# Kernel tuning notes

Measured on AMD Instinct MI355X. Metric: run time of the kernel, lower is better.

## Reference

```python
import jax, jax.numpy as jnp
import numpy as np

USER_NUM = 100_000
ITEM_NUM = 50_000
N = USER_NUM + ITEM_NUM          # total nodes in the bipartite graph
HIDDEN = 64
LAYERS = 3
BATCH = 4096
NNZ = 4_800_000                  # ~avg degree 32


def setup_inputs() -> dict:
    key = jax.random.key(0)
    ks = jax.random.split(key, 7)
    emb = jax.random.normal(ks[0], (N, HIDDEN), dtype=jnp.float32) * 0.02
    rows = jax.random.randint(ks[1], (NNZ,), 0, N, dtype=jnp.int32)
    cols = jax.random.randint(ks[2], (NNZ,), 0, N, dtype=jnp.int32)
    # normalized-laplacian-like positive values, scaled ~ 1/avg_degree
    vals = jax.random.uniform(ks[3], (NNZ,), dtype=jnp.float32) * (1.0 / 32.0)
    user = jax.random.randint(ks[4], (BATCH,), 0, USER_NUM, dtype=jnp.int32)
    pos = jax.random.randint(ks[5], (BATCH,), USER_NUM, N, dtype=jnp.int32)
    neg = jax.random.randint(ks[6], (BATCH,), USER_NUM, N, dtype=jnp.int32)
    return {"emb": emb, "vals": vals, "rows": rows, "cols": cols,
            "user": user, "pos": pos, "neg": neg}


def _spmm(rows, cols, vals, x):
    # sparse [N,N] @ dense [N,d] in COO form: gather + scale + segment-sum
    return jax.ops.segment_sum(vals[:, None] * x[cols], rows, num_segments=N)


def reference(emb, vals, rows, cols, user, pos, neg):
    # layer-0 gathers
    user_acc = emb[user]
    pos_acc = emb[pos]
    neg_acc = emb[neg]
    e = emb
    for _ in range(LAYERS):
        e = _spmm(rows, cols, vals, e)
        user_acc = user_acc + e[user]
        pos_acc = pos_acc + e[pos]
        neg_acc = neg_acc + e[neg]
    denom = jnp.float32(LAYERS + 1)
    u = user_acc / denom   # mean over stacked layers
    p = pos_acc / denom
    n = neg_acc / denom
    pos_logits = jnp.einsum('id,id->i', u, p)
    neg_logits = jnp.einsum('id,id->i', u, n)
    # -log(sigmoid(x)) == -log_sigmoid(x) (numerically stable)
    loss = -jax.nn.log_sigmoid(pos_logits - neg_logits)
    return loss.sum()
```

## Files before the change

kernel.cpp:

```cpp
#include <hip/hip_runtime.h>

#define HIDDEN 64
#define PAD 96
#define CHUNK 8192
#define NBMAX 640
#define CAP 9600

typedef unsigned int uint;

__device__ __forceinline__ ushort f2bf(float f) {
    uint u = __float_as_uint(f);
    u = (u + 0x7FFFu + ((u >> 16) & 1u)) >> 16;
    return (ushort)u;
}
__device__ __forceinline__ float bf2f(ushort h) {
    return __uint_as_float(((uint)h) << 16);
}


__global__ void __launch_bounds__(256) k_f2bf(const float4* __restrict__ src,
                                              ushort* __restrict__ dst, int n4) {
    int i = blockIdx.x * blockDim.x + threadIdx.x;
    if (i >= n4) return;
    float4 f = src[i];
    ushort4 o;
    o.x = f2bf(f.x); o.y = f2bf(f.y); o.z = f2bf(f.z); o.w = f2bf(f.w);
    ((ushort4*)dst)[i] = o;
}


__global__ void __launch_bounds__(512) k_stage(const int* __restrict__ rows,
                                               const int* __restrict__ cols,
                                               const float* __restrict__ vals,
                                               int* __restrict__ cursor,
                                               int2* __restrict__ staged,
                                               int nnz, int nb) {
    __shared__ int  hS[NBMAX];
    __shared__ int  lsS[NBMAX];
    __shared__ int  gsS[NBMAX];
    __shared__ int  lcS[NBMAX];
    __shared__ int  ps[512];
    __shared__ int2 stg[CHUNK];

    int t  = threadIdx.x;
    int cb = blockIdx.x * CHUNK;

    for (int k = t; k < nb; k += 512) hS[k] = 0;
    __syncthreads();

    int4 ra[4];
    #pragma unroll
    for (int j = 0; j < 4; ++j) {
        int idx = cb + j * 2048 + t * 4;
        int4 r4;
        if (idx + 3 < nnz) {
            r4 = *(const int4*)(rows + idx);
        } else {
            r4.x = (idx     < nnz) ? rows[idx]     : -1;
            r4.y = (idx + 1 < nnz) ? rows[idx + 1] : -1;
            r4.z = (idx + 2 < nnz) ? rows[idx + 2] : -1;
            r4.w = (idx + 3 < nnz) ? rows[idx + 3] : -1;
        }
        ra[j] = r4;
        if (r4.x >= 0) atomicAdd(&hS[r4.x >> 8], 1);
        if (r4.y >= 0) atomicAdd(&hS[r4.y >> 8], 1);
        if (r4.z >= 0) atomicAdd(&hS[r4.z >> 8], 1);
        if (r4.w >= 0) atomicAdd(&hS[r4.w >> 8], 1);
    }
    __syncthreads();

    int k0 = 2 * t, k1 = 2 * t + 1;
    int c0 = (k0 < nb) ? hS[k0] : 0;
    int c1 = (k1 < nb) ? hS[k1] : 0;
    ps[t] = c0 + c1;
    __syncthreads();
    for (int d = 1; d < 512; d <<= 1) {
        int p = (t >= d) ? ps[t - d] : 0;
        __syncthreads();
        ps[t] += p;
        __syncthreads();
    }
    int excl = ps[t] - (c0 + c1);
    if (k0 < nb) {
        lsS[k0] = excl;
        gsS[k0] = atomicAdd(&cursor[k0], c0);
    }
    if (k1 < nb) {
        lsS[k1] = excl + c0;
        gsS[k1] = atomicAdd(&cursor[k1], c1);
    }
    __syncthreads();
    for (int k = t; k < nb; k += 512) lcS[k] = lsS[k];
    __syncthreads();

    #pragma unroll
    for (int j = 0; j < 4; ++j) {
        int idx = cb + j * 2048 + t * 4;
        int4 r4 = ra[j];
        int4 c4; float4 v4;
        if (idx + 3 < nnz) {
            c4 = *(const int4*)(cols + idx);
            v4 = *(const float4*)(vals + idx);
        } else {
            c4.x = (idx     < nnz) ? cols[idx]     : 0;
            c4.y = (idx + 1 < nnz) ? cols[idx + 1] : 0;
            c4.z = (idx + 2 < nnz) ? cols[idx + 2] : 0;
            c4.w = (idx + 3 < nnz) ? cols[idx + 3] : 0;
            v4.x = (idx     < nnz) ? vals[idx]     : 0.f;
            v4.y = (idx + 1 < nnz) ? vals[idx + 1] : 0.f;
            v4.z = (idx + 2 < nnz) ? vals[idx + 2] : 0.f;
            v4.w = (idx + 3 < nnz) ? vals[idx + 3] : 0.f;
        }
        if (r4.x >= 0) { int s = atomicAdd(&lcS[r4.x >> 8], 1);
            stg[s] = make_int2(c4.x | ((r4.x & 255) << 18), __float_as_int(v4.x)); }
        if (r4.y >= 0) { int s = atomicAdd(&lcS[r4.y >> 8], 1);
            stg[s] = make_int2(c4.y | ((r4.y & 255) << 18), __float_as_int(v4.y)); }
        if (r4.z >= 0) { int s = atomicAdd(&lcS[r4.z >> 8], 1);
            stg[s] = make_int2(c4.z | ((r4.z & 255) << 18), __float_as_int(v4.z)); }
        if (r4.w >= 0) { int s = atomicAdd(&lcS[r4.w >> 8], 1);
            stg[s] = make_int2(c4.w | ((r4.w & 255) << 18), __float_as_int(v4.w)); }
    }
    __syncthreads();

    int m_total = nnz - cb; if (m_total > CHUNK) m_total = CHUNK;
    for (int i = t; i < m_total; i += 512) {
        int2 e = stg[i];
        int lo = 0, hi = nb - 1;
        while (lo < hi) {
            int mid = (lo + hi + 1) >> 1;
            if (lsS[mid] <= i) lo = mid; else hi = mid - 1;
        }
        int k = lo;
        int pos = gsS[k] + (i - lsS[k]);
        if (pos < CAP) staged[(size_t)k * CAP + pos] = e;
    }
}

__global__ void __launch_bounds__(1024) k_fine(const int2* __restrict__ staged,
                                               const int* __restrict__ stagecnt,
                                               int2* __restrict__ pack,
                                               int* __restrict__ cnt, int n) {
    __shared__ int2 out[CAP];
    __shared__ int hist[256], rstart[256], cursor[256], s2[256];
    int k = blockIdx.x;
    int t = threadIdx.x;
    size_t s0 = (size_t)k * CAP;
    int ck = stagecnt[k]; if (ck > CAP) ck = CAP;
    if (t < 256) hist[t] = 0;
    __syncthreads();
    for (int i = t; i < ck; i += 1024)
        atomicAdd(&hist[((uint)staged[s0 + i].x) >> 18], 1);
    __syncthreads();
    if (t < 256) s2[t] = hist[t];
    __syncthreads();
    for (int d = 1; d < 256; d <<= 1) {
        int p = (t < 256 && t >= d) ? s2[t - d] : 0;
        __syncthreads();
        if (t < 256) s2[t] += p;
        __syncthreads();
    }
    if (t < 256) {
        int rs = s2[t] - hist[t];
        rstart[t] = rs;
        cursor[t] = rs;
        int row = (k << 8) + t;
        if (row < n) cnt[row] = hist[t];
    }
    __syncthreads();
    for (int i = t; i < ck; i += 1024) {
        int2 e = staged[s0 + i];
        int lr = ((uint)e.x) >> 18;
        int slot = atomicAdd(&cursor[lr], 1);
        if (slot < CAP) out[slot] = make_int2(e.x & 0x3FFFF, e.y);
    }
    __syncthreads();
    for (int idx = t; idx < 256 * PAD; idx += 1024) {
        int lr = idx / PAD, j = idx - lr * PAD;
        if (j < hist[lr]) {
            int row = (k << 8) + lr;
            pack[(size_t)row * PAD + j] = out[rstart[lr] + j];
        }
    }
}


__device__ __forceinline__ float4 spmm_row4(const int* __restrict__ cnt,
                                            const int2* __restrict__ pack,
                                            const ushort* __restrict__ x,
                                            int row, int lane) {
    int len = cnt[row]; if (len > PAD) len = PAD;
    const int2* base = pack + (size_t)row * PAD;
    int g = (lane & 15) * 4;
    int e = lane >> 4;
    float a0 = 0.f, a1 = 0.f, a2 = 0.f, a3 = 0.f;
    float b0 = 0.f, b1 = 0.f, b2 = 0.f, b3 = 0.f;
    for (int j0 = 0; j0 < len; j0 += 64) {
        int m = len - j0; if (m > 64) m = 64;
        int c = 0; float v = 0.f;
        if (lane < m) {
            int2 cv = base[j0 + lane];
            c = cv.x;
            v = __int_as_float(cv.y);
        }
        int steps = (m + 3) >> 2;
        int s = 0;
        for (; s + 1 < steps; s += 2) {
            int   i0 = 4 * s + e,  i1 = 4 * s + 4 + e;
            int   c0 = __shfl(c, i0); float v0 = __shfl(v, i0);
            int   c1 = __shfl(c, i1); float v1 = __shfl(v, i1);
            ushort4 x0 = *(const ushort4*)(x + (size_t)c0 * HIDDEN + g);
            ushort4 x1 = *(const ushort4*)(x + (size_t)c1 * HIDDEN + g);
            a0 += v0 * bf2f(x0.x); a1 += v0 * bf2f(x0.y);
            a2 += v0 * bf2f(x0.z); a3 += v0 * bf2f(x0.w);
            b0 += v1 * bf2f(x1.x); b1 += v1 * bf2f(x1.y);
            b2 += v1 * bf2f(x1.z); b3 += v1 * bf2f(x1.w);
        }
        if (s < steps) {
            int i0 = 4 * s + e;
            int c0 = __shfl(c, i0); float v0 = __shfl(v, i0);
            ushort4 x0 = *(const ushort4*)(x + (size_t)c0 * HIDDEN + g);
            a0 += v0 * bf2f(x0.x); a1 += v0 * bf2f(x0.y);
            a2 += v0 * bf2f(x0.z); a3 += v0 * bf2f(x0.w);
        }
    }
    a0 += b0; a1 += b1; a2 += b2; a3 += b3;
    a0 += __shfl_xor(a0, 16); a1 += __shfl_xor(a1, 16);
    a2 += __shfl_xor(a2, 16); a3 += __shfl_xor(a3, 16);
    a0 += __shfl_xor(a0, 32); a1 += __shfl_xor(a1, 32);
    a2 += __shfl_xor(a2, 32); a3 += __shfl_xor(a3, 32);
    return make_float4(a0, a1, a2, a3);
}

__global__ void __launch_bounds__(256) k_spmm(const int* __restrict__ cnt,
                                              const int2* __restrict__ pack,
                                              const ushort* __restrict__ x,
                                              ushort* __restrict__ y, int n) {
    int row  = (int)((blockIdx.x * blockDim.x + threadIdx.x) >> 6);
    int lane = threadIdx.x & 63;
    if (row >= n) return;
    float4 a = spmm_row4(cnt, pack, x, row, lane);
    if (lane < 16) {
        ushort4 o;
        o.x = f2bf(a.x); o.y = f2bf(a.y); o.z = f2bf(a.z); o.w = f2bf(a.w);
        *(ushort4*)(y + (size_t)row * HIDDEN + lane * 4) = o;
    }
}

__global__ void __launch_bounds__(256) k_spmm_batch(const int* __restrict__ cnt,
                                                    const int2* __restrict__ pack,
                                                    const ushort* __restrict__ x,
                                                    const int* __restrict__ user,
                                                    const int* __restrict__ pos,
                                                    const int* __restrict__ neg,
                                                    int batch, float* __restrict__ acc) {
    int slot = (int)((blockIdx.x * blockDim.x + threadIdx.x) >> 6);
    int lane = threadIdx.x & 63;
    if (slot >= 3 * batch) return;
    int which = slot / batch, i = slot - which * batch;
    const int* sel = (which == 0) ? user : (which == 1 ? pos : neg);
    float4 a = spmm_row4(cnt, pack, x, sel[i], lane);
    if (lane < 16) {
        float4* p = (float4*)(acc + (size_t)slot * HIDDEN + lane * 4);
        float4 old = *p;
        old.x += a.x; old.y += a.y; old.z += a.z; old.w += a.w;
        *p = old;
    }
}


__global__ void __launch_bounds__(256) k_gather0(const float* __restrict__ e,
                                                 const int* __restrict__ user,
                                                 const int* __restrict__ pos,
                                                 const int* __restrict__ neg,
                                                 int batch, float* __restrict__ acc) {
    int row  = (int)((blockIdx.x * blockDim.x + threadIdx.x) >> 6);
    int lane = threadIdx.x & 63;
    if (row >= 3 * batch) return;
    int which = row / batch, i = row - which * batch;
    const int* sel = (which == 0) ? user : (which == 1 ? pos : neg);
    int s = sel[i];
    acc[(size_t)row * HIDDEN + lane] = e[(size_t)s * HIDDEN + lane];
}

__global__ void __launch_bounds__(256) k_gather_bf(const ushort* __restrict__ e,
                                                   const int* __restrict__ user,
                                                   const int* __restrict__ pos,
                                                   const int* __restrict__ neg,
                                                   int batch, float* __restrict__ acc) {
    int row  = (int)((blockIdx.x * blockDim.x + threadIdx.x) >> 6);
    int lane = threadIdx.x & 63;
    if (row >= 3 * batch) return;
    int which = row / batch, i = row - which * batch;
    const int* sel = (which == 0) ? user : (which == 1 ? pos : neg);
    int s = sel[i];
    acc[(size_t)row * HIDDEN + lane] += bf2f(e[(size_t)s * HIDDEN + lane]);
}


__global__ void __launch_bounds__(256) k_loss(const float* __restrict__ acc, int batch,
                                              float* __restrict__ out) {
    int i    = (int)((blockIdx.x * blockDim.x + threadIdx.x) >> 6);
    int lane = threadIdx.x & 63;
    if (i >= batch) return;
    float u  = acc[(size_t)i * HIDDEN + lane] * 0.25f;
    float p  = acc[(size_t)(i + batch) * HIDDEN + lane] * 0.25f;
    float nn = acc[(size_t)(i + 2 * batch) * HIDDEN + lane] * 0.25f;
    float sp = u * p, sn = u * nn;
    for (int d = 32; d > 0; d >>= 1) {
        sp += __shfl_down(sp, d);
        sn += __shfl_down(sn, d);
    }
    if (lane == 0) {
        float z = sn - sp;
        float loss = fmaxf(z, 0.f) + log1pf(expf(-fabsf(z)));
        atomicAdd(out, loss);
    }
}


extern "C" void kernel_launch(void* const* d_in, const int* in_sizes, int n_in,
                              void* d_out, int out_size, void* d_ws, size_t ws_size,
                              hipStream_t stream) {
    (void)n_in; (void)out_size; (void)ws_size;
    const float* emb  = (const float*)d_in[0];
    const float* vals = (const float*)d_in[1];
    const int*   rows = (const int*)d_in[2];
    const int*   cols = (const int*)d_in[3];
    const int*   user = (const int*)d_in[4];
    const int*   pos  = (const int*)d_in[5];
    const int*   neg  = (const int*)d_in[6];

    const int n     = in_sizes[0] / HIDDEN;
    const int nnz   = in_sizes[1];
    const int batch = in_sizes[4];

    const int nb   = (n + 255) >> 8;
    const int nblk = (nnz + CHUNK - 1) / CHUNK;

    auto align256 = [](size_t x) { return (x + 255) & ~(size_t)255; };
    char* w = (char*)d_ws;
    int*    cnt    = (int*)w;    w += align256(sizeof(int)  * (size_t)n);
    int*    cursor = (int*)w;    w += align256(sizeof(int)  * (size_t)NBMAX);
    int2*   pack   = (int2*)w;   w += align256(sizeof(int2) * (size_t)n * PAD);
    ushort* emb_bf = (ushort*)w; w += align256(sizeof(ushort) * (size_t)n * HIDDEN);
    ushort* e0     = (ushort*)w; w += align256(sizeof(ushort) * (size_t)n * HIDDEN);
    ushort* e1     = (ushort*)w; w += align256(sizeof(ushort) * (size_t)n * HIDDEN);
    float*  acc    = (float*)w;  w += align256(sizeof(float)  * (size_t)3 * batch * HIDDEN);
    int2*   stg_x  = (int2*)w;   w += align256(sizeof(int2) * ((size_t)nb * CAP > 3u * n * HIDDEN ?
                                               (size_t)nb * CAP - 3u * n * HIDDEN : 0));

    int2* staged = (int2*)emb_bf;
    (void)stg_x;

    float* out = (float*)d_out;

    const int B = 256;
    dim3 blk(B);
    int g_conv  = (n * HIDDEN / 4 + B - 1) / B;
    int g_spmm  = (n + 3) / 4;
    int g_gath  = (3 * batch + 3) / 4;
    int g_loss  = (batch + 3) / 4;

    hipMemsetAsync(cursor, 0, sizeof(int) * (size_t)NBMAX, stream);
    k_stage<<<nblk, 512, 0, stream>>>(rows, cols, vals, cursor, staged, nnz, nb);
    k_fine<<<nb, 1024, 0, stream>>>(staged, cursor, pack, cnt, n);

    k_f2bf<<<g_conv, blk, 0, stream>>>((const float4*)emb, emb_bf, n * HIDDEN / 4);

    hipMemsetAsync(out, 0, sizeof(float), stream);

    k_gather0<<<g_gath, blk, 0, stream>>>(emb, user, pos, neg, batch, acc);
    k_spmm<<<g_spmm, blk, 0, stream>>>(cnt, pack, emb_bf, e0, n);
    k_gather_bf<<<g_gath, blk, 0, stream>>>(e0, user, pos, neg, batch, acc);
    k_spmm<<<g_spmm, blk, 0, stream>>>(cnt, pack, e0, e1, n);
    k_gather_bf<<<g_gath, blk, 0, stream>>>(e1, user, pos, neg, batch, acc);
    k_spmm_batch<<<g_gath, blk, 0, stream>>>(cnt, pack, e1, user, pos, neg, batch, acc);

    k_loss<<<g_loss, blk, 0, stream>>>(acc, batch, out);
}
```

Baseline: 348.4 us.

## Store embeddings in scaled FP8 and split ELL into int cols plus bf16 vals

Intermediate layer embeddings move from bf16 to FP8 (e4m3 via hardware conversion builtins when available), with a fixed scale of 64 applied before encoding and undone on accumulation. The ELL structure is split into separate int column and bf16 value arrays instead of int2 pairs. The gather kernel packs four rows per wavefront. The aim is to halve the bytes moved by the random row gathers in SpMM and cut index/value traffic, at the cost of much lower precision in the propagated embeddings and edge weights, which may break the accuracy tolerance.

```diff
diff --git a/kernel.cpp b/kernel.cpp
--- a/kernel.cpp
+++ b/kernel.cpp
@@ -5,8 +5,11 @@
 #define CHUNK 8192
 #define NBMAX 640
 #define CAP 9600
+#define S_SCALE 64.0f
+#define INV_S 0.015625f
 
 typedef unsigned int uint;
+typedef unsigned char uchar;
 
 __device__ __forceinline__ ushort f2bf(float f) {
     uint u = __float_as_uint(f);
@@ -17,15 +20,61 @@
     return __uint_as_float(((uint)h) << 16);
 }
 
-
-__global__ void __launch_bounds__(256) k_f2bf(const float4* __restrict__ src,
-                                              ushort* __restrict__ dst, int n4) {
+#if __has_builtin(__builtin_amdgcn_cvt_pk_fp8_f32) && __has_builtin(__builtin_amdgcn_cvt_pk_f32_fp8)
+#define FP8_HW 1
+#else
+#define FP8_HW 0
+#endif
+
+__device__ __forceinline__ uint enc8(float a, float b, float c, float d) {
+#if FP8_HW
+    int r = __builtin_amdgcn_cvt_pk_fp8_f32(a, b, 0, false);
+    r = __builtin_amdgcn_cvt_pk_fp8_f32(c, d, r, true);
+    return (uint)r;
+#else
+    auto enc1 = [](float x) -> uint {
+        uint u = __float_as_uint(x);
+        uint s = (u >> 24) & 0x80u;
+        float af = fabsf(x);
+        if (af < 0.015625f) return s;
+        if (af >= 448.f) return s | 0x7Eu;
+        uint bits = u & 0x7FFFFFFFu;
+        bits -= (120u << 23);
+        uint r = (bits + 0x7FFFFu + ((bits >> 20) & 1u)) >> 20;
+        if (r > 0x7Eu) r = 0x7Eu;
+        return s | r;
+    };
+    return enc1(a) | (enc1(b) << 8) | (enc1(c) << 16) | (enc1(d) << 24);
+#endif
+}
+
+__device__ __forceinline__ float4 dec8(uint u) {
+#if FP8_HW
+    auto lo = __builtin_amdgcn_cvt_pk_f32_fp8((int)u, false);
+    auto hi = __builtin_amdgcn_cvt_pk_f32_fp8((int)u, true);
+    return make_float4(lo[0], lo[1], hi[0], hi[1]);
+#else
+    auto dec1 = [](uint b) -> float {
+        uint m = b & 0x7Fu;
+        uint s = (b & 0x80u) << 24;
+        uint bits = m ? (s | ((m + 960u) << 20)) : s;
+        return __uint_as_float(bits);
+    };
+    return make_float4(dec1(u & 0xFF), dec1((u >> 8) & 0xFF),
+                       dec1((u >> 16) & 0xFF), dec1((u >> 24) & 0xFF));
+#endif
+}
+
+
+__global__ void __launch_bounds__(256) k_f2fp8(const float4* __restrict__ src,
+                                               uint2* __restrict__ dst, int n8) {
     int i = blockIdx.x * blockDim.x + threadIdx.x;
-    if (i >= n4) return;
-    float4 f = src[i];
-    ushort4 o;
-    o.x = f2bf(f.x); o.y = f2bf(f.y); o.z = f2bf(f.z); o.w = f2bf(f.w);
-    ((ushort4*)dst)[i] = o;
+    if (i >= n8) return;
+    float4 f0 = src[2 * i], f1 = src[2 * i + 1];
+    uint2 o;
+    o.x = enc8(f0.x * S_SCALE, f0.y * S_SCALE, f0.z * S_SCALE, f0.w * S_SCALE);
+    o.y = enc8(f1.x * S_SCALE, f1.y * S_SCALE, f1.z * S_SCALE, f1.w * S_SCALE);
+    dst[i] = o;
 }
 
 
@@ -81,14 +130,8 @@
         __syncthreads();
     }
     int excl = ps[t] - (c0 + c1);
-    if (k0 < nb) {
-        lsS[k0] = excl;
-        gsS[k0] = atomicAdd(&cursor[k0], c0);
-    }
-    if (k1 < nb) {
-        lsS[k1] = excl + c0;
-        gsS[k1] = atomicAdd(&cursor[k1], c1);
-    }
+    if (k0 < nb) { lsS[k0] = excl;      gsS[k0] = atomicAdd(&cursor[k0], c0); }
+    if (k1 < nb) { lsS[k1] = excl + c0; gsS[k1] = atomicAdd(&cursor[k1], c1); }
     __syncthreads();
     for (int k = t; k < nb; k += 512) lcS[k] = lsS[k];
     __syncthreads();
@@ -138,7 +181,8 @@
 
 __global__ void __launch_bounds__(1024) k_fine(const int2* __restrict__ staged,
                                                const int* __restrict__ stagecnt,
-                                               int2* __restrict__ pack,
+                                               int* __restrict__ cols_ell,
+                                               ushort* __restrict__ vals_ell,
                                                int* __restrict__ cnt, int n) {
     __shared__ int2 out[CAP];
     __shared__ int hist[256], rstart[256], cursor[256], s2[256];
@@ -178,19 +222,23 @@
         int lr = idx / PAD, j = idx - lr * PAD;
         if (j < hist[lr]) {
             int row = (k << 8) + lr;
-            pack[(size_t)row * PAD + j] = out[rstart[lr] + j];
+            int2 o = out[rstart[lr] + j];
+            cols_ell[(size_t)row * PAD + j] = o.x;
+            vals_ell[(size_t)row * PAD + j] = f2bf(__int_as_float(o.y));
         }
     }
 }
 
 
 __device__ __forceinline__ float4 spmm_row4(const int* __restrict__ cnt,
-                                            const int2* __restrict__ pack,
-                                            const ushort* __restrict__ x,
+                                            const int* __restrict__ cols_ell,
+                                            const ushort* __restrict__ vals_ell,
+                                            const uchar* __restrict__ x,
                                             int row, int lane) {
     int len = cnt[row]; if (len > PAD) len = PAD;
-    const int2* base = pack + (size_t)row * PAD;
-    int g = (lane & 15) * 4;
+    const int*    cbp = cols_ell + (size_t)row * PAD;
+    const ushort* vbp = vals_ell + (size_t)row * PAD;
+    int g4 = (lane & 15) * 4;
     int e = lane >> 4;
     float a0 = 0.f, a1 = 0.f, a2 = 0.f, a3 = 0.f;
     float b0 = 0.f, b1 = 0.f, b2 = 0.f, b3 = 0.f;
@@ -198,9 +246,8 @@
         int m = len - j0; if (m > 64) m = 64;
         int c = 0; float v = 0.f;
         if (lane < m) {
-            int2 cv = base[j0 + lane];
-            c = cv.x;
-            v = __int_as_float(cv.y);
+            c = cbp[j0 + lane];
+            v = bf2f(vbp[j0 + lane]);
         }
         int steps = (m + 3) >> 2;
         int s = 0;
@@ -208,19 +255,19 @@
             int   i0 = 4 * s + e,  i1 = 4 * s + 4 + e;
             int   c0 = __shfl(c, i0); float v0 = __shfl(v, i0);
             int   c1 = __shfl(c, i1); float v1 = __shfl(v, i1);
-            ushort4 x0 = *(const ushort4*)(x + (size_t)c0 * HIDDEN + g);
-            ushort4 x1 = *(const ushort4*)(x + (size_t)c1 * HIDDEN + g);
-            a0 += v0 * bf2f(x0.x); a1 += v0 * bf2f(x0.y);
-            a2 += v0 * bf2f(x0.z); a3 += v0 * bf2f(x0.w);
-            b0 += v1 * bf2f(x1.x); b1 += v1 * bf2f(x1.y);
-            b2 += v1 * bf2f(x1.z); b3 += v1 * bf2f(x1.w);
+            uint u0 = *(const uint*)(x + ((size_t)c0 << 6) + g4);
+            uint u1 = *(const uint*)(x + ((size_t)c1 << 6) + g4);
+            float4 x0 = dec8(u0);
+            float4 x1 = dec8(u1);
+            a0 += v0 * x0.x; a1 += v0 * x0.y; a2 += v0 * x0.z; a3 += v0 * x0.w;
+            b0 += v1 * x1.x; b1 += v1 * x1.y; b2 += v1 * x1.z; b3 += v1 * x1.w;
         }
         if (s < steps) {
             int i0 = 4 * s + e;
             int c0 = __shfl(c, i0); float v0 = __shfl(v, i0);
-            ushort4 x0 = *(const ushort4*)(x + (size_t)c0 * HIDDEN + g);
-            a0 += v0 * bf2f(x0.x); a1 += v0 * bf2f(x0.y);
-            a2 += v0 * bf2f(x0.z); a3 += v0 * bf2f(x0.w);
+            uint u0 = *(const uint*)(x + ((size_t)c0 << 6) + g4);
+            float4 x0 = dec8(u0);
+            a0 += v0 * x0.x; a1 += v0 * x0.y; a2 += v0 * x0.z; a3 += v0 * x0.w;
         }
     }
     a0 += b0; a1 += b1; a2 += b2; a3 += b3;
@@ -232,23 +279,24 @@
 }
 
 __global__ void __launch_bounds__(256) k_spmm(const int* __restrict__ cnt,
-                                              const int2* __restrict__ pack,
-                                              const ushort* __restrict__ x,
-                                              ushort* __restrict__ y, int n) {
+                                              const int* __restrict__ cols_ell,
+                                              const ushort* __restrict__ vals_ell,
+                                              const uchar* __restrict__ x,
+                                              uchar* __restrict__ y, int n) {
     int row  = (int)((blockIdx.x * blockDim.x + threadIdx.x) >> 6);
     int lane = threadIdx.x & 63;
     if (row >= n) return;
-    float4 a = spmm_row4(cnt, pack, x, row, lane);
+    float4 a = spmm_row4(cnt, cols_ell, vals_ell, x, row, lane);
     if (lane < 16) {
-        ushort4 o;
-        o.x = f2bf(a.x); o.y = f2bf(a.y); o.z = f2bf(a.z); o.w = f2bf(a.w);
-        *(ushort4*)(y + (size_t)row * HIDDEN + lane * 4) = o;
+        uint r = enc8(a.x, a.y, a.z, a.w);
+        *(uint*)(y + ((size_t)row << 6) + lane * 4) = r;
     }
 }
 
 __global__ void __launch_bounds__(256) k_spmm_batch(const int* __restrict__ cnt,
-                                                    const int2* __restrict__ pack,
-                                                    const ushort* __restrict__ x,
+                                                    const int* __restrict__ cols_ell,
+                                                    const ushort* __restrict__ vals_ell,
+                                                    const uchar* __restrict__ x,
                                                     const int* __restrict__ user,
                                                     const int* __restrict__ pos,
                                                     const int* __restrict__ neg,
@@ -258,11 +306,12 @@
     if (slot >= 3 * batch) return;
     int which = slot / batch, i = slot - which * batch;
     const int* sel = (which == 0) ? user : (which == 1 ? pos : neg);
-    float4 a = spmm_row4(cnt, pack, x, sel[i], lane);
+    float4 a = spmm_row4(cnt, cols_ell, vals_ell, x, sel[i], lane);
     if (lane < 16) {
         float4* p = (float4*)(acc + (size_t)slot * HIDDEN + lane * 4);
         float4 old = *p;
-        old.x += a.x; old.y += a.y; old.z += a.z; old.w += a.w;
+        old.x += a.x * INV_S; old.y += a.y * INV_S;
+        old.z += a.z * INV_S; old.w += a.w * INV_S;
         *p = old;
     }
 }
@@ -282,18 +331,27 @@
     acc[(size_t)row * HIDDEN + lane] = e[(size_t)s * HIDDEN + lane];
 }
 
-__global__ void __launch_bounds__(256) k_gather_bf(const ushort* __restrict__ e,
-                                                   const int* __restrict__ user,
-                                                   const int* __restrict__ pos,
-                                                   const int* __restrict__ neg,
-                                                   int batch, float* __restrict__ acc) {
-    int row  = (int)((blockIdx.x * blockDim.x + threadIdx.x) >> 6);
+__global__ void __launch_bounds__(256) k_gather8(const uchar* __restrict__ e,
+                                                 const int* __restrict__ user,
+                                                 const int* __restrict__ pos,
+                                                 const int* __restrict__ neg,
+                                                 int batch, float* __restrict__ acc) {
+    int t    = blockIdx.x * blockDim.x + threadIdx.x;
+    int wv   = t >> 6;
     int lane = threadIdx.x & 63;
+    int row  = wv * 4 + (lane >> 4);
     if (row >= 3 * batch) return;
     int which = row / batch, i = row - which * batch;
     const int* sel = (which == 0) ? user : (which == 1 ? pos : neg);
     int s = sel[i];
-    acc[(size_t)row * HIDDEN + lane] += bf2f(e[(size_t)s * HIDDEN + lane]);
+    int g4 = (lane & 15) * 4;
+    uint u = *(const uint*)(e + ((size_t)s << 6) + g4);
+    float4 d = dec8(u);
+    float4* p = (float4*)(acc + (size_t)row * HIDDEN + g4);
+    float4 old = *p;
+    old.x += d.x * INV_S; old.y += d.y * INV_S;
+    old.z += d.z * INV_S; old.w += d.w * INV_S;
+    *p = old;
 }
 
 
@@ -339,42 +397,40 @@
 
     auto align256 = [](size_t x) { return (x + 255) & ~(size_t)255; };
     char* w = (char*)d_ws;
-    int*    cnt    = (int*)w;    w += align256(sizeof(int)  * (size_t)n);
-    int*    cursor = (int*)w;    w += align256(sizeof(int)  * (size_t)NBMAX);
-    int2*   pack   = (int2*)w;   w += align256(sizeof(int2) * (size_t)n * PAD);
-    ushort* emb_bf = (ushort*)w; w += align256(sizeof(ushort) * (size_t)n * HIDDEN);
-    ushort* e0     = (ushort*)w; w += align256(sizeof(ushort) * (size_t)n * HIDDEN);
-    ushort* e1     = (ushort*)w; w += align256(sizeof(ushort) * (size_t)n * HIDDEN);
-    float*  acc    = (float*)w;  w += align256(sizeof(float)  * (size_t)3 * batch * HIDDEN);
-    int2*   stg_x  = (int2*)w;   w += align256(sizeof(int2) * ((size_t)nb * CAP > 3u * n * HIDDEN ?
-                                               (size_t)nb * CAP - 3u * n * HIDDEN : 0));
-
-    int2* staged = (int2*)emb_bf;
-    (void)stg_x;
+    int*    cnt      = (int*)w;    w += align256(sizeof(int)    * (size_t)n);
+    int*    cursor   = (int*)w;    w += align256(sizeof(int)    * (size_t)NBMAX);
+    int*    cols_ell = (int*)w;    w += align256(sizeof(int)    * (size_t)n * PAD);
+    ushort* vals_ell = (ushort*)w; w += align256(sizeof(ushort) * (size_t)n * PAD);
+    uchar*  emb8     = (uchar*)w;  w += align256((size_t)n * HIDDEN);
+    uchar*  e0       = (uchar*)w;  w += align256((size_t)n * HIDDEN);
+    uchar*  e1       = (uchar*)w;  w += align256((size_t)n * HIDDEN);
+    float*  acc      = (float*)w;  w += align256(sizeof(float)  * (size_t)3 * batch * HIDDEN);
+    int2*   staged   = (int2*)w;   w += align256(sizeof(int2)   * (size_t)nb * CAP);
 
     float* out = (float*)d_out;
 
     const int B = 256;
     dim3 blk(B);
-    int g_conv  = (n * HIDDEN / 4 + B - 1) / B;
-    int g_spmm  = (n + 3) / 4;
-    int g_gath  = (3 * batch + 3) / 4;
-    int g_loss  = (batch + 3) / 4;
+    int g_conv = (n * HIDDEN / 8 + B - 1) / B;
+    int g_spmm = (n + 3) / 4;
+    int g_gath = (3 * batch + 3) / 4;
+    int g_g8   = ((3 * batch + 3) / 4 * 64 + B - 1) / B;
+    int g_loss = (batch + 3) / 4;
 
     hipMemsetAsync(cursor, 0, sizeof(int) * (size_t)NBMAX, stream);
     k_stage<<<nblk, 512, 0, stream>>>(rows, cols, vals, cursor, staged, nnz, nb);
-    k_fine<<<nb, 1024, 0, stream>>>(staged, cursor, pack, cnt, n);
-
-    k_f2bf<<<g_conv, blk, 0, stream>>>((const float4*)emb, emb_bf, n * HIDDEN / 4);
+    k_fine<<<nb, 1024, 0, stream>>>(staged, cursor, cols_ell, vals_ell, cnt, n);
+
+    k_f2fp8<<<g_conv, blk, 0, stream>>>((const float4*)emb, (uint2*)emb8, n * HIDDEN / 8);
 
     hipMemsetAsync(out, 0, sizeof(float), stream);
 
     k_gather0<<<g_gath, blk, 0, stream>>>(emb, user, pos, neg, batch, acc);
-    k_spmm<<<g_spmm, blk, 0, stream>>>(cnt, pack, emb_bf, e0, n);
-    k_gather_bf<<<g_gath, blk, 0, stream>>>(e0, user, pos, neg, batch, acc);
-    k_spmm<<<g_spmm, blk, 0, stream>>>(cnt, pack, e0, e1, n);
-    k_gather_bf<<<g_gath, blk, 0, stream>>>(e1, user, pos, neg, batch, acc);
-    k_spmm_batch<<<g_gath, blk, 0, stream>>>(cnt, pack, e1, user, pos, neg, batch, acc);
+    k_spmm<<<g_spmm, blk, 0, stream>>>(cnt, cols_ell, vals_ell, emb8, e0, n);
+    k_gather8<<<g_g8, blk, 0, stream>>>(e0, user, pos, neg, batch, acc);
+    k_spmm<<<g_spmm, blk, 0, stream>>>(cnt, cols_ell, vals_ell, e0, e1, n);
+    k_gather8<<<g_g8, blk, 0, stream>>>(e1, user, pos, neg, batch, acc);
+    k_spmm_batch<<<g_gath, blk, 0, stream>>>(cnt, cols_ell, vals_ell, e1, user, pos, neg, batch, acc);
 
     k_loss<<<g_loss, blk, 0, stream>>>(acc, batch, out);
 }
```

After: 325.0 us. 1.07x faster.
